# Kernel tuning notes

Hardware: AMD Instinct MI355X
Metric: run time of the kernel (lower is better)

The kernel has to match this reference:

```python
import math
import jax, jax.numpy as jnp
import numpy as np
from jax import lax

B, T, D = 2, 2048, 1024
H, W, E = 16, 16, 8
HD = D // H


def setup_inputs() -> dict:
    key = jax.random.key(0)
    ks = jax.random.split(key, 9)
    s = 0.02
    return {
        "x": jax.random.normal(ks[0], (B, T, D), dtype=jnp.float32),
        # CausalConv1d weights: torch Conv1d layout [out_ch, in_ch, kernel]
        "q_w": jax.random.normal(ks[1], (D, D, W), dtype=jnp.float32) * s,
        "q_b": jax.random.normal(ks[2], (D,), dtype=jnp.float32) * s,
        "k_w": jax.random.normal(ks[3], (D, D, W), dtype=jnp.float32) * s,
        "k_b": jax.random.normal(ks[4], (D,), dtype=jnp.float32) * s,
        # Linear weights: torch layout [out, in]
        "v_w": jax.random.normal(ks[5], (D, D), dtype=jnp.float32) * s,
        "v_b": jax.random.normal(ks[6], (D,), dtype=jnp.float32) * s,
        "p_w": jax.random.normal(ks[7], (D, D), dtype=jnp.float32) * s,
        "p_b": jax.random.normal(ks[8], (D,), dtype=jnp.float32) * s,
    }


def _causal_conv(x_t, w, b):
    # x_t: [B, D, T]; left-pad by W-1 so output at t sees inputs <= t
    xp = jnp.pad(x_t, ((0, 0), (0, 0), (W - 1, 0)))
    y = lax.conv_general_dilated(xp, w, window_strides=(1,), padding="VALID",
                                 dimension_numbers=("NCH", "OIH", "NCH"))
    return y + b[None, :, None]


def _split_heads(z):
    # [B, T, D] -> [B, H, T, hd]
    return z.reshape(B, T, H, HD).transpose(0, 2, 1, 3)


def reference(x, q_w, q_b, k_w, k_b, v_w, v_b, p_w, p_b):
    x_t = x.transpose(0, 2, 1)  # [B, D, T]
    q = _split_heads(_causal_conv(x_t, q_w, q_b).transpose(0, 2, 1))
    k = _split_heads(_causal_conv(x_t, k_w, k_b).transpose(0, 2, 1))
    v = _split_heads(jnp.einsum("btd,od->bto", x, v_w) + v_b)
    scale = 1.0 / math.sqrt(HD)

    # ---- local window attention (unfold equivalent) ----
    # zero-pad keys/values W-1 steps to the left along T, gather sliding windows
    k_pad = jnp.pad(k, ((0, 0), (0, 0), (W - 1, 0), (0, 0)))
    v_pad = jnp.pad(v, ((0, 0), (0, 0), (W - 1, 0), (0, 0)))
    widx = jnp.arange(T)[:, None] + jnp.arange(W)[None, :]  # [T, W]
    patches_k = k_pad[:, :, widx]  # [B, H, T, W, hd]
    patches_v = v_pad[:, :, widx]  # [B, H, T, W, hd]
    attn_l = jax.nn.softmax(jnp.einsum("bhtd,bhtwd->bhtw", q, patches_k) * scale, axis=-1)
    out_l = jnp.einsum("bhtw,bhtwd->bhtd", attn_l, patches_v)

    # ---- exponential jumps: roll by 2^e (wrap-around, as in original) ----
    out_e = jnp.zeros_like(out_l)
    for e in range(E):
        shift = 2 ** e
        if shift >= T:
            break
        k_s = jnp.roll(k, -shift, axis=2)
        v_s = jnp.roll(v, -shift, axis=2)
        score = jnp.sum(q * k_s, axis=-1) * scale  # [B, H, T]
        alpha = jax.nn.softmax(score, axis=-1)[..., None]  # softmax over T (faithful)
        out_e = out_e + alpha * v_s

    out = (out_l + out_e).transpose(0, 2, 1, 3).reshape(B, T, D)
    return jnp.einsum("btd,od->bto", out, p_w) + p_b
```

## Files before the change

kernel.cpp:

```cpp
#include <hip/hip_runtime.h>
#include <cstdint>
#include <cstddef>

#define TSEQ 2048
#define DDIM 1024

typedef _Float16 f16;
typedef _Float16 f16x2 __attribute__((ext_vector_type(2)));
typedef _Float16 f16x4 __attribute__((ext_vector_type(4)));
typedef _Float16 f16x8 __attribute__((ext_vector_type(8)));
typedef float f32x4 __attribute__((ext_vector_type(4)));


__device__ __align__(16) static const unsigned char g_zero16[16] = {};

__device__ __forceinline__ void gload_lds16(const void* g, void* l) {
  __builtin_amdgcn_global_load_lds(
      (const __attribute__((address_space(1))) void*)g,
      (__attribute__((address_space(3))) void*)l, 16, 0, 0);
}

__global__ void cvt_all(const float* __restrict__ x, const float* __restrict__ vw,
                        const float* __restrict__ pw,
                        f16* __restrict__ xh, f16* __restrict__ vwh, f16* __restrict__ pwh) {
  int b = blockIdx.x;
  const float* src; f16* dst; int i;
  if (b < 4096)      { src = x;  dst = xh;  i = b * 256 + threadIdx.x; }
  else if (b < 5120) { src = vw; dst = vwh; i = (b - 4096) * 256 + threadIdx.x; }
  else               { src = pw; dst = pwh; i = (b - 5120) * 256 + threadIdx.x; }
  float4 v = ((const float4*)src)[i];
  f16x4 h = { (f16)v.x, (f16)v.y, (f16)v.z, (f16)v.w };
  ((f16x4*)dst)[i] = h;
}

__global__ __launch_bounds__(256) void cvt_w_frag(const float* __restrict__ qw,
                                                  const float* __restrict__ kw,
                                                  f16* __restrict__ qd, f16* __restrict__ kd) {
  extern __shared__ f16 wt_lds[];
  const int bid = blockIdx.x;
  const float* src; f16* dst;
  int o0;
  if (bid < 256) { src = qw; dst = qd; o0 = bid * 4; }
  else           { src = kw; dst = kd; o0 = (bid - 256) * 4; }
  const int tid = threadIdx.x;
  for (int p = 0; p < 64; p++) {
    const int idx = p * 256 + tid;
    const int ro = idx >> 12;
    const int rem = idx & 4095;
    const int i = rem >> 2, wq2 = rem & 3;
    float4 v = *(const float4*)(src + (size_t)(o0 + ro) * 16384 + (size_t)i * 16 + wq2 * 4);
    f16* trow = wt_lds + ro * 16512 + i;
    trow[(wq2 * 4 + 0) * 1032] = (f16)v.x;
    trow[(wq2 * 4 + 1) * 1032] = (f16)v.y;
    trow[(wq2 * 4 + 2) * 1032] = (f16)v.z;
    trow[(wq2 * 4 + 3) * 1032] = (f16)v.w;
  }
  __syncthreads();
  const int jj = (o0 >> 4) & 3;
  const int nb = o0 >> 6;
  for (int p8 = 0; p8 < 8; p8++) {
    const int p = p8 * 256 + tid;
    const int ktp = p >> 3;
    const int s = (p >> 2) & 1;
    const int lhi = p & 3;
    const int w = ktp & 15;
    const int ibb = ktp >> 4;
    const int i0 = ibb * 64 + s * 32 + lhi * 8;
    const size_t dbase = (((size_t)(nb * 256 + ktp)) * 8 + jj * 2 + s) * 512;
    #pragma unroll
    for (int ro = 0; ro < 4; ro++) {
      const int l = lhi * 16 + ((o0 + ro) & 15);
      *(f16x8*)(dst + dbase + l * 8) =
          *(const f16x8*)&wt_lds[ro * 16512 + w * 1032 + i0];
    }
  }
}

__global__ __launch_bounds__(512, 1) void gemm_qk8(
    const f16* __restrict__ xh,
    const f16* __restrict__ Wfq, const f16* __restrict__ Wfk,
    const float* __restrict__ bq, const float* __restrict__ bk,
    f16* __restrict__ oq, f16* __restrict__ ok)
{
  extern __shared__ __align__(16) f16 smem[];
  const int tid = threadIdx.x;
  const int lane = tid & 63;
  const int wid = tid >> 6;
  const int wq = wid >> 1;
  const int wp = wid & 1;

  const int flat = blockIdx.y * 16 + blockIdx.x;
  const int xcd = flat & 7;
  const int idx = flat >> 3;
  const int nblk = xcd * 2 + (idx >> 4);
  const int mblk = idx & 15;
  const int m0 = mblk * 256;
  const int n0 = nblk * 64;
  const int bT = m0 & ~(TSEQ - 1);
  const int t0 = m0 & (TSEQ - 1);

  const int srow = lane >> 3;
  const int chunk8 = (((lane & 7) ^ (srow & 7)) << 3);

  const f16* Wf = wp ? Wfk : Wfq;
  const f16* wbase = Wf + ((size_t)nblk << 20) + lane * 8;

  f32x4 acc[4][4] = {};
  f16x8 bfr[2][8];

  auto stageX = [&](int ib2, int bufp) {
    f16* sb = smem + bufp * 17408;
    const int ic = ib2 * 64 + chunk8;
    #pragma unroll
    for (int c = 0; c < 5; c++) {
      const int g = c * 8 + wid;
      if (g < 34) {
        const int srcT = t0 + g * 8 + srow - 15;
        const void* gp = (srcT >= 0)
            ? (const void*)(xh + (((size_t)(bT + srcT)) << 10) + ic)
            : (const void*)g_zero16;
        gload_lds16(gp, (void*)&sb[g * 512]);
      }
    }
  };

  auto loadB = [&](int kt, f16x8* bf) {
    const f16* p = wbase + ((size_t)kt << 12);
    #pragma unroll
    for (int f = 0; f < 8; f++)
      bf[f] = *(const f16x8*)(p + f * 512);
  };

  stageX(0, 0);
  loadB(0, bfr[0]);
  asm volatile("s_waitcnt vmcnt(0)" ::: "memory");
  __builtin_amdgcn_s_barrier();
  __builtin_amdgcn_sched_barrier(0);

  for (int ib = 0; ib < 16; ib++) {
    if (ib > 0) {
      __builtin_amdgcn_s_barrier();
      __builtin_amdgcn_sched_barrier(0);
    }
    if (ib + 1 < 16) stageX(ib + 1, (ib + 1) & 1);
    __builtin_amdgcn_sched_barrier(0);
    const f16* xb = smem + (ib & 1) * 17408;
    #pragma unroll
    for (int wt = 0; wt < 16; wt++) {
      const int kt = ib * 16 + wt;
      const int rx = ((lane & 7) + wt) & 7;
      const int sl0 = (((lane >> 4)) ^ rx) << 3;
      const int sl1 = (((lane >> 4) + 4) ^ rx) << 3;
      f16x8 af[8];
      #pragma unroll
      for (int i = 0; i < 4; i++) {
        const int row = wq * 64 + i * 16 + (lane & 15) + wt;
        af[i]     = *(const f16x8*)&xb[row * 64 + sl0];
        af[4 + i] = *(const f16x8*)&xb[row * 64 + sl1];
      }
      if (kt + 1 < 256) loadB(kt + 1, bfr[(wt & 1) ^ 1]);
      __builtin_amdgcn_s_setprio(1);
      #pragma unroll
      for (int i = 0; i < 4; i++)
        #pragma unroll
        for (int j = 0; j < 4; j++)
          acc[i][j] = __builtin_amdgcn_mfma_f32_16x16x32_f16(
              af[i], bfr[wt & 1][2 * j], acc[i][j], 0, 0, 0);
      #pragma unroll
      for (int i = 0; i < 4; i++)
        #pragma unroll
        for (int j = 0; j < 4; j++)
          acc[i][j] = __builtin_amdgcn_mfma_f32_16x16x32_f16(
              af[4 + i], bfr[wt & 1][2 * j + 1], acc[i][j], 0, 0, 0);
      __builtin_amdgcn_s_setprio(0);
    }
  }

  const int crow = (lane >> 4) << 2;
  const int ccol = lane & 15;
  const int hh = n0 >> 6;
  const float* bias = wp ? bk : bq;
  f16* outp = wp ? ok : oq;
  #pragma unroll
  for (int j = 0; j < 4; j++) {
    const int col = n0 + j * 16 + ccol;
    const float bvl = bias[col];
    const int d = (j << 4) + ccol;
    #pragma unroll
    for (int i = 0; i < 4; i++) {
      #pragma unroll
      for (int r = 0; r < 4; r++) {
        const int row = m0 + wq * 64 + i * 16 + crow + r;
        const int b = row >> 11, t = row & (TSEQ - 1);
        outp[((size_t)(b * 16 + hh) * TSEQ + t) * 64 + d] = (f16)(acc[i][j][r] + bvl);
      }
    }
  }
}

template<int MODE>
__global__ __launch_bounds__(256, 2) void gemm_small(
    const f16* __restrict__ A, const f16* __restrict__ Bw,
    const float* __restrict__ bias, f16* __restrict__ oh, float* __restrict__ ofp)
{
  __shared__ f16 As[128 * 32];
  __shared__ f16 Bs[128 * 32];
  const int tid = threadIdx.x;
  const int lane = tid & 63;
  const int wid = tid >> 6;
  const int m0 = blockIdx.x * 128;
  const int n0 = blockIdx.y * 128;

  const int srow = lane >> 2;
  const int scg = ((lane & 3) ^ ((lane >> 3) & 3)) * 8;
  const int wm = wid & 1;
  const int wn = wid >> 1;

  f32x4 acc[4][4] = {};

  for (int kk = 0; kk < 1024; kk += 32) {
    __syncthreads();
    if (wid < 2) {
      #pragma unroll
      for (int c = 0; c < 4; c++) {
        const int r = wid * 64 + c * 16 + srow;
        const void* g = (const void*)(A + (((size_t)(m0 + r)) << 10) + kk + scg);
        gload_lds16(g, (void*)&As[(wid * 64 + c * 16) * 32]);
      }
    } else {
      #pragma unroll
      for (int c = 0; c < 4; c++) {
        const int r = (wid - 2) * 64 + c * 16 + srow;
        const void* g = (const void*)(Bw + (((size_t)(n0 + r)) << 10) + kk + scg);
        gload_lds16(g, (void*)&Bs[((wid - 2) * 64 + c * 16) * 32]);
      }
    }
    __syncthreads();
    const int koff = ((lane >> 4) ^ ((lane >> 1) & 3)) * 8;
    f16x8 af[4], bf[4];
    #pragma unroll
    for (int i = 0; i < 4; i++) {
      af[i] = *(const f16x8*)&As[(wm * 64 + i * 16 + (lane & 15)) * 32 + koff];
      bf[i] = *(const f16x8*)&Bs[(wn * 64 + i * 16 + (lane & 15)) * 32 + koff];
    }
    #pragma unroll
    for (int i = 0; i < 4; i++)
      #pragma unroll
      for (int j = 0; j < 4; j++)
        acc[i][j] = __builtin_amdgcn_mfma_f32_16x16x32_f16(af[i], bf[j], acc[i][j], 0, 0, 0);
  }

  const int crow = (lane >> 4) * 4;
  const int ccol = lane & 15;
  #pragma unroll
  for (int j = 0; j < 4; j++) {
    const int col = n0 + wn * 64 + j * 16 + ccol;
    const float bvl = bias[col];
    #pragma unroll
    for (int i = 0; i < 4; i++) {
      #pragma unroll
      for (int r = 0; r < 4; r++) {
        const int row = m0 + wm * 64 + i * 16 + crow + r;
        const float val = acc[i][j][r] + bvl;
        if (MODE == 1) {
          ofp[(size_t)row * DDIM + col] = val;
        } else {
          const int b = row >> 11, t = row & (TSEQ - 1);
          const int h = col >> 6, d = col & 63;
          oh[((size_t)(b * 16 + h) * TSEQ + t) * 64 + d] = (f16)val;
        }
      }
    }
  }
}

__global__ __launch_bounds__(256) void score_k(const f16* __restrict__ qh,
                                               const f16* __restrict__ kh,
                                               float* __restrict__ scores) {
  const int bid = blockIdx.x;
  const int bh = bid >> 5, tc = bid & 31;
  const int tid = threadIdx.x;
  const int wave = tid >> 6, lane = tid & 63;
  const int tr = lane >> 3, dc = lane & 7;
  const size_t base = ((size_t)bh) << 17;
  const f16* qb = qh + base;
  const f16* kb = kh + base;

  #pragma unroll
  for (int p = 0; p < 2; p++) {
    const int t = tc * 64 + p * 32 + wave * 8 + tr;
    f16x8 qv = *(const f16x8*)(qb + (size_t)t * 64 + dc * 8);
    const f16x2* qp = (const f16x2*)&qv;
    #pragma unroll
    for (int e = 0; e < 8; e++) {
      const int ts = (t + (1 << e)) & (TSEQ - 1);
      f16x8 kv = *(const f16x8*)(kb + (size_t)ts * 64 + dc * 8);
      const f16x2* kp = (const f16x2*)&kv;
      float s = 0.f;
      #pragma unroll
      for (int j = 0; j < 4; j++) s = __builtin_amdgcn_fdot2(qp[j], kp[j], s, false);
      s += __shfl_xor(s, 1, 64);
      s += __shfl_xor(s, 2, 64);
      s += __shfl_xor(s, 4, 64);
      if (dc == 0) scores[((size_t)(bh * 8 + e) << 11) + t] = s * 0.125f;
    }
  }
}

__global__ void softmax_k(float* __restrict__ scores) {
  __shared__ float red[4];
  int row = blockIdx.x;
  float* p = scores + ((size_t)row << 11);
  int tid = threadIdx.x;
  float v[8];
  float4 a = ((const float4*)p)[tid * 2];
  float4 b = ((const float4*)p)[tid * 2 + 1];
  v[0] = a.x; v[1] = a.y; v[2] = a.z; v[3] = a.w;
  v[4] = b.x; v[5] = b.y; v[6] = b.z; v[7] = b.w;
  float m = v[0];
  #pragma unroll
  for (int j = 1; j < 8; j++) m = fmaxf(m, v[j]);
  for (int o = 32; o > 0; o >>= 1) m = fmaxf(m, __shfl_xor(m, o, 64));
  if ((tid & 63) == 0) red[tid >> 6] = m;
  __syncthreads();
  m = fmaxf(fmaxf(red[0], red[1]), fmaxf(red[2], red[3]));
  __syncthreads();
  float s = 0.f;
  #pragma unroll
  for (int j = 0; j < 8; j++) { v[j] = __expf(v[j] - m); s += v[j]; }
  for (int o = 32; o > 0; o >>= 1) s += __shfl_xor(s, o, 64);
  if ((tid & 63) == 0) red[tid >> 6] = s;
  __syncthreads();
  s = (red[0] + red[1]) + (red[2] + red[3]);
  float inv = 1.0f / s;
  float4 o1 = make_float4(v[0] * inv, v[1] * inv, v[2] * inv, v[3] * inv);
  float4 o2 = make_float4(v[4] * inv, v[5] * inv, v[6] * inv, v[7] * inv);
  ((float4*)p)[tid * 2] = o1;
  ((float4*)p)[tid * 2 + 1] = o2;
}

__global__ __launch_bounds__(256) void attn_out_k(
    const f16* __restrict__ qh, const f16* __restrict__ kh, const f16* __restrict__ vh,
    const float* __restrict__ alpha, f16* __restrict__ outh)
{
  __shared__ f16 qL[64 * 64];
  __shared__ f16 kL[80 * 64];
  __shared__ f16 vL[208 * 64];
  __shared__ float scL[64 * 16];
  __shared__ float aL[8 * 64];
  const int bh = blockIdx.x, tc = blockIdx.y;
  const int t0 = tc * 64;
  const int tid = threadIdx.x;
  const size_t base = ((size_t)bh) << 17;

  for (int idx = tid; idx < 64 * 8; idx += 256) {
    int r = idx >> 3, c = idx & 7, sl = c ^ (r & 7);
    *(uint4*)&qL[r * 64 + sl * 8] = *(const uint4*)(qh + base + (size_t)(t0 + r) * 64 + c * 8);
  }
  for (int idx = tid; idx < 79 * 8; idx += 256) {
    int r = idx >> 3, c = idx & 7, sl = c ^ (r & 7);
    int g = t0 - 15 + r;
    uint4 val = (g < 0) ? make_uint4(0, 0, 0, 0)
                        : *(const uint4*)(kh + base + (size_t)g * 64 + c * 8);
    *(uint4*)&kL[r * 64 + sl * 8] = val;
  }
  for (int idx = tid; idx < 207 * 8; idx += 256) {
    int r = idx >> 3, c = idx & 7, sl = c ^ (r & 7);
    int g = t0 - 15 + r;
    uint4 val;
    if (g < 0) val = make_uint4(0, 0, 0, 0);
    else {
      if (g >= TSEQ) g -= TSEQ;
      val = *(const uint4*)(vh + base + (size_t)g * 64 + c * 8);
    }
    *(uint4*)&vL[r * 64 + sl * 8] = val;
  }
  for (int idx = tid; idx < 512; idx += 256) {
    int e = idx >> 6, i = idx & 63;
    aL[e * 64 + i] = alpha[((size_t)(bh * 8 + e) << 11) + t0 + i];
  }
  __syncthreads();

  {
    const int tl = tid & 63;
    const int wg = tid >> 6;
    f16x8 qv[8];
    #pragma unroll
    for (int c = 0; c < 8; c++) qv[c] = *(const f16x8*)&qL[tl * 64 + ((c ^ (tl & 7)) * 8)];
    const f16x2* qp = (const f16x2*)&qv[0];
    #pragma unroll
    for (int wi = 0; wi < 4; wi++) {
      const int w = wg * 4 + wi;
      const int r = tl + w;
      float s = 0.f;
      #pragma unroll
      for (int c = 0; c < 8; c++) {
        f16x8 kv = *(const f16x8*)&kL[r * 64 + ((c ^ (r & 7)) * 8)];
        const f16x2* kp = (const f16x2*)&kv;
        #pragma unroll
        for (int j = 0; j < 4; j++) s = __builtin_amdgcn_fdot2(qp[c * 4 + j], kp[j], s, false);
      }
      scL[tl * 16 + w] = s * 0.125f;
    }
  }
  __syncthreads();

  if (tid < 64) {
    float sc[16];
    float m = -1e30f;
    #pragma unroll
    for (int w = 0; w < 16; w++) { sc[w] = scL[tid * 16 + w]; m = fmaxf(m, sc[w]); }
    float sum = 0.f;
    #pragma unroll
    for (int w = 0; w < 16; w++) { sc[w] = __expf(sc[w] - m); sum += sc[w]; }
    float inv = 1.0f / sum;
    #pragma unroll
    for (int w = 0; w < 16; w++) scL[tid * 16 + w] = sc[w] * inv;
  }
  __syncthreads();

  {
    const int tl = tid >> 2;
    const int qd = tid & 3;
    float accv[16] = {};
    #pragma unroll
    for (int w = 0; w < 16; w++) {
      const float pw_ = scL[tl * 16 + w];
      const int r = tl + w;
      #pragma unroll
      for (int c2 = 0; c2 < 2; c2++) {
        const int c = qd * 2 + c2;
        f16x8 v = *(const f16x8*)&vL[r * 64 + ((c ^ (r & 7)) * 8)];
        #pragma unroll
        for (int j = 0; j < 8; j++) accv[c2 * 8 + j] += pw_ * (float)v[j];
      }
    }
    #pragma unroll
    for (int e = 0; e < 8; e++) {
      const float a = aL[e * 64 + tl];
      const int r = tl + 15 + (1 << e);
      #pragma unroll
      for (int c2 = 0; c2 < 2; c2++) {
        const int c = qd * 2 + c2;
        f16x8 v = *(const f16x8*)&vL[r * 64 + ((c ^ (r & 7)) * 8)];
        #pragma unroll
        for (int j = 0; j < 8; j++) accv[c2 * 8 + j] += a * (float)v[j];
      }
    }
    const int b = bh >> 4, h = bh & 15;
    f16* orow = outh + ((size_t)(b * TSEQ + t0 + tl)) * DDIM + h * 64 + qd * 16;
    #pragma unroll
    for (int c2 = 0; c2 < 2; c2++) {
      f16x8 v;
      #pragma unroll
      for (int j = 0; j < 8; j++) v[j] = (f16)accv[c2 * 8 + j];
      *(f16x8*)(orow + c2 * 8) = v;
    }
  }
}

extern "C" void kernel_launch(void* const* d_in, const int* in_sizes, int n_in,
                              void* d_out, int out_size, void* d_ws, size_t ws_size,
                              hipStream_t stream) {
  (void)in_sizes; (void)n_in; (void)out_size; (void)ws_size;
  const float* x   = (const float*)d_in[0];
  const float* q_w = (const float*)d_in[1];
  const float* q_b = (const float*)d_in[2];
  const float* k_w = (const float*)d_in[3];
  const float* k_b = (const float*)d_in[4];
  const float* v_w = (const float*)d_in[5];
  const float* v_b = (const float*)d_in[6];
  const float* p_w = (const float*)d_in[7];
  const float* p_b = (const float*)d_in[8];
  float* out = (float*)d_out;

  char* ws = (char*)d_ws;
  f16* xh      = (f16*)(ws);
  f16* qwh     = (f16*)(ws + 8388608);
  f16* kwh     = (f16*)(ws + 41943040);
  f16* vwh     = (f16*)(ws + 75497472);
  f16* pwh     = (f16*)(ws + 77594624);
  f16* qh      = (f16*)(ws + 79691776);
  f16* kh      = (f16*)(ws + 88080384);
  f16* vh      = (f16*)(ws + 96468992);
  f16* outh    = (f16*)(ws + 104857600);
  float* alpha = (float*)(ws + 113246208);

  static int s_attr_done = 0;
  if (!s_attr_done) {
    hipFuncSetAttribute((const void*)gemm_qk8,
                        hipFuncAttributeMaxDynamicSharedMemorySize, 69632);
    hipFuncSetAttribute((const void*)cvt_w_frag,
                        hipFuncAttributeMaxDynamicSharedMemorySize, 132096);
    s_attr_done = 1;
  }

  cvt_all<<<6144, 256, 0, stream>>>(x, v_w, p_w, xh, vwh, pwh);
  cvt_w_frag<<<512, 256, 132096, stream>>>(q_w, k_w, qwh, kwh);

  gemm_qk8<<<dim3(16, 16), 512, 69632, stream>>>(xh, qwh, kwh, q_b, k_b, qh, kh);
  gemm_small<0><<<dim3(32, 8), 256, 0, stream>>>(xh, vwh, v_b, vh, nullptr);

  score_k<<<1024, 256, 0, stream>>>(qh, kh, alpha);
  softmax_k<<<256, 256, 0, stream>>>(alpha);
  attn_out_k<<<dim3(32, 32), 256, 0, stream>>>(qh, kh, vh, alpha, outh);

  gemm_small<1><<<dim3(32, 8), 256, 0, stream>>>(outh, pwh, p_b, nullptr, out);
}
```

Measured before the change: 488.9 us.

## Retile weight fragment conversion and double-buffer A-fragment LDS reads in QK GEMM

The conv-weight conversion kernel is retiled so each block handles 16 output rows by 128 input channels with an XOR-swizzled LDS transpose. This halves shared memory per block, doubles the grid, and cuts bank conflicts. The QK GEMM now prefetches the next window's A fragments from LDS into a second register buffer while the current MFMAs run. The cost is higher register pressure in a kernel already launched at one block per CU.

```diff
diff --git a/kernel.cpp b/kernel.cpp
--- a/kernel.cpp
+++ b/kernel.cpp
@@ -38,41 +38,47 @@
                                                   f16* __restrict__ qd, f16* __restrict__ kd) {
   extern __shared__ f16 wt_lds[];
   const int bid = blockIdx.x;
-  const float* src; f16* dst;
-  int o0;
-  if (bid < 256) { src = qw; dst = qd; o0 = bid * 4; }
-  else           { src = kw; dst = kd; o0 = (bid - 256) * 4; }
+  const int proj = bid >> 9;
+  const int nb = (bid >> 5) & 15;
+  const int j = (bid >> 3) & 3;
+  const int ic = bid & 7;
+  const float* src = proj ? kw : qw;
+  f16* dst = proj ? kd : qd;
+  const int o_base = nb * 64 + j * 16;
   const int tid = threadIdx.x;
-  for (int p = 0; p < 64; p++) {
-    const int idx = p * 256 + tid;
-    const int ro = idx >> 12;
-    const int rem = idx & 4095;
-    const int i = rem >> 2, wq2 = rem & 3;
-    float4 v = *(const float4*)(src + (size_t)(o0 + ro) * 16384 + (size_t)i * 16 + wq2 * 4);
-    f16* trow = wt_lds + ro * 16512 + i;
-    trow[(wq2 * 4 + 0) * 1032] = (f16)v.x;
-    trow[(wq2 * 4 + 1) * 1032] = (f16)v.y;
-    trow[(wq2 * 4 + 2) * 1032] = (f16)v.z;
-    trow[(wq2 * 4 + 3) * 1032] = (f16)v.w;
-  }
-  __syncthreads();
-  const int jj = (o0 >> 4) & 3;
-  const int nb = o0 >> 6;
-  for (int p8 = 0; p8 < 8; p8++) {
-    const int p = p8 * 256 + tid;
-    const int ktp = p >> 3;
-    const int s = (p >> 2) & 1;
-    const int lhi = p & 3;
-    const int w = ktp & 15;
-    const int ibb = ktp >> 4;
-    const int i0 = ibb * 64 + s * 32 + lhi * 8;
-    const size_t dbase = (((size_t)(nb * 256 + ktp)) * 8 + jj * 2 + s) * 512;
-    #pragma unroll
-    for (int ro = 0; ro < 4; ro++) {
-      const int l = lhi * 16 + ((o0 + ro) & 15);
-      *(f16x8*)(dst + dbase + l * 8) =
-          *(const f16x8*)&wt_lds[ro * 16512 + w * 1032 + i0];
-    }
+  const int lane = tid & 63;
+  const int wv = tid >> 6;
+
+  #pragma unroll
+  for (int p = 0; p < 32; p++) {
+    const int gidx = p * 256 + tid;
+    const int o_r = gidx >> 9;
+    const int i_r = (gidx >> 2) & 127;
+    const int wq2 = gidx & 3;
+    float4 v = *(const float4*)(src + (size_t)(o_base + o_r) * 16384 +
+                                (size_t)(ic * 128 + i_r) * 16 + wq2 * 4);
+    const int g = i_r >> 3;
+    const int gp = (g & 8) | ((g & 7) ^ (o_r & 7));
+    const int ip = gp * 8 + (i_r & 7);
+    f16* t0 = wt_lds + ((wq2 * 4) * 16 + o_r) * 130 + ip;
+    t0[0]    = (f16)v.x;
+    t0[2080] = (f16)v.y;
+    t0[4160] = (f16)v.z;
+    t0[6240] = (f16)v.w;
+  }
+  __syncthreads();
+
+  const int o = lane & 15;
+  const int lhi = lane >> 4;
+  #pragma unroll
+  for (int u4 = 0; u4 < 16; u4++) {
+    const int u = u4 * 4 + wv;
+    const int w = u >> 2, ih = (u >> 1) & 1, s = u & 1;
+    const int gl = ih * 8 + s * 4 + lhi;
+    const int gp = (gl & 8) | ((gl & 7) ^ (o & 7));
+    f16x8 val = *(const f16x8*)&wt_lds[(w * 16 + o) * 130 + gp * 8];
+    const size_t unit = ((size_t)(nb * 256 + (ic * 2 + ih) * 16 + w) * 8) + j * 2 + s;
+    *(f16x8*)(dst + unit * 512 + lane * 8) = val;
   }
 }
 
@@ -107,6 +113,7 @@
 
   f32x4 acc[4][4] = {};
   f16x8 bfr[2][8];
+  f16x8 afr[2][8];
 
   auto stageX = [&](int ib2, int bufp) {
     f16* sb = smem + bufp * 17408;
@@ -131,6 +138,18 @@
       bf[f] = *(const f16x8*)(p + f * 512);
   };
 
+  auto readA = [&](const f16* xb, int wt, f16x8* af) {
+    const int rx = ((lane & 7) + wt) & 7;
+    const int sl0 = (((lane >> 4)) ^ rx) << 3;
+    const int sl1 = (((lane >> 4) + 4) ^ rx) << 3;
+    #pragma unroll
+    for (int i = 0; i < 4; i++) {
+      const int row = wq * 64 + i * 16 + (lane & 15) + wt;
+      af[i]     = *(const f16x8*)&xb[row * 64 + sl0];
+      af[4 + i] = *(const f16x8*)&xb[row * 64 + sl1];
+    }
+  };
+
   stageX(0, 0);
   loadB(0, bfr[0]);
   asm volatile("s_waitcnt vmcnt(0)" ::: "memory");
@@ -145,19 +164,11 @@
     if (ib + 1 < 16) stageX(ib + 1, (ib + 1) & 1);
     __builtin_amdgcn_sched_barrier(0);
     const f16* xb = smem + (ib & 1) * 17408;
+    readA(xb, 0, afr[0]);
     #pragma unroll
     for (int wt = 0; wt < 16; wt++) {
+      if (wt < 15) readA(xb, wt + 1, afr[(wt + 1) & 1]);
       const int kt = ib * 16 + wt;
-      const int rx = ((lane & 7) + wt) & 7;
-      const int sl0 = (((lane >> 4)) ^ rx) << 3;
-      const int sl1 = (((lane >> 4) + 4) ^ rx) << 3;
-      f16x8 af[8];
-      #pragma unroll
-      for (int i = 0; i < 4; i++) {
-        const int row = wq * 64 + i * 16 + (lane & 15) + wt;
-        af[i]     = *(const f16x8*)&xb[row * 64 + sl0];
-        af[4 + i] = *(const f16x8*)&xb[row * 64 + sl1];
-      }
       if (kt + 1 < 256) loadB(kt + 1, bfr[(wt & 1) ^ 1]);
       __builtin_amdgcn_s_setprio(1);
       #pragma unroll
@@ -165,13 +176,13 @@
         #pragma unroll
         for (int j = 0; j < 4; j++)
           acc[i][j] = __builtin_amdgcn_mfma_f32_16x16x32_f16(
-              af[i], bfr[wt & 1][2 * j], acc[i][j], 0, 0, 0);
+              afr[wt & 1][i], bfr[wt & 1][2 * j], acc[i][j], 0, 0, 0);
       #pragma unroll
       for (int i = 0; i < 4; i++)
         #pragma unroll
         for (int j = 0; j < 4; j++)
           acc[i][j] = __builtin_amdgcn_mfma_f32_16x16x32_f16(
-              af[4 + i], bfr[wt & 1][2 * j + 1], acc[i][j], 0, 0, 0);
+              afr[wt & 1][4 + i], bfr[wt & 1][2 * j + 1], acc[i][j], 0, 0, 0);
       __builtin_amdgcn_s_setprio(0);
     }
   }
@@ -491,12 +502,12 @@
     hipFuncSetAttribute((const void*)gemm_qk8,
                         hipFuncAttributeMaxDynamicSharedMemorySize, 69632);
     hipFuncSetAttribute((const void*)cvt_w_frag,
-                        hipFuncAttributeMaxDynamicSharedMemorySize, 132096);
+                        hipFuncAttributeMaxDynamicSharedMemorySize, 66560);
     s_attr_done = 1;
   }
 
   cvt_all<<<6144, 256, 0, stream>>>(x, v_w, p_w, xh, vwh, pwh);
-  cvt_w_frag<<<512, 256, 132096, stream>>>(q_w, k_w, qwh, kwh);
+  cvt_w_frag<<<1024, 256, 66560, stream>>>(q_w, k_w, qwh, kwh);
 
   gemm_qk8<<<dim3(16, 16), 512, 69632, stream>>>(xh, qwh, kwh, q_b, k_b, qh, kh);
   gemm_small<0><<<dim3(32, 8), 256, 0, stream>>>(xh, vwh, v_b, vh, nullptr);
```

Result: slower. 509.2 us (+4.1%).
